# Performance work log

Measured on AMD Instinct MI355X. Metric: run time of the kernel, lower is better.

The kernel has to match this reference:

```python
import jax, jax.numpy as jnp
import numpy as np

VERTEX_W = 1.0
SMOOTH_W = 0.1
SYM_W = 0.05
CHAMFER_W = 0.1

B, N = 4, 8192  # N points per cloud, flat dim = N*3


def setup_inputs() -> dict:
    key = jax.random.key(0)
    k1, k2 = jax.random.split(key)
    pred = jax.random.normal(k1, (B, N * 3), dtype=jnp.float32)
    targ = jax.random.normal(k2, (B, N * 3), dtype=jnp.float32)
    return {"pred_vertices": pred, "target_vertices": targ}


def _chamfer(x, y):
    # x: [B,N,3], y: [B,M,3]; euclidean cdist via matmul expansion
    x2 = jnp.sum(x * x, axis=-1)  # [B,N]
    y2 = jnp.sum(y * y, axis=-1)  # [B,M]
    xy = jnp.einsum('bnd,bmd->bnm', x, y)  # [B,N,M]
    d2 = x2[:, :, None] + y2[None if False else slice(None), None, :] - 2.0 * xy
    d = jnp.sqrt(jnp.maximum(d2, 0.0))
    return jnp.mean(jnp.min(d, axis=2)) + jnp.mean(jnp.min(d, axis=1))


def reference(pred_vertices, target_vertices):
    b = pred_vertices.shape[0]
    pv = pred_vertices.reshape(b, -1, 3)
    tv = target_vertices.reshape(b, -1, 3)

    # vertex MSE (on flat tensors, same as mse on reshaped)
    vertex_loss = jnp.mean((pred_vertices - target_vertices) ** 2)

    # smoothness: mean L2 norm of consecutive vertex diffs
    diff = pv[:, 1:, :] - pv[:, :-1, :]
    smoothness_loss = jnp.mean(jnp.linalg.norm(diff, axis=2))

    # symmetry: N is even in this config
    mid = pv.shape[1] // 2
    left = pv[:, :mid, :]
    right = jnp.flip(pv[:, mid:, :], axis=1)
    right = right.at[:, :, 0].multiply(-1.0)
    symmetry_loss = jnp.mean((left - right) ** 2)

    chamfer_loss = _chamfer(pv, tv)

    total = (VERTEX_W * vertex_loss + SMOOTH_W * smoothness_loss
             + SYM_W * symmetry_loss + CHAMFER_W * chamfer_loss)
    return total
```

## Files before the change

kernel.cpp:

```cpp
#include <hip/hip_runtime.h>
#include <hip/hip_bf16.h>


#define B_ 4
#define N_ 8192
#define MID_ (N_ / 2)
#define CNT_OFF 1536
#define RP_OFF 1664
#define PM_OFF 4096
#define PACK_OFF (PM_OFF + 4 * 2 * B_ * N_)
#define PACK_STRIDE (B_ * N_ * 16)

typedef short short8 __attribute__((ext_vector_type(8)));
typedef float f32x16 __attribute__((ext_vector_type(16)));

__global__ void AdvancedLoss3D_1881195675843_kernel() {}

__device__ inline unsigned short bfu(float x) {
    union { __hip_bfloat16 b; unsigned short u; } c;
    c.b = __float2bfloat16(x);
    return c.u;
}
__device__ inline float bff(unsigned short u) {
    union { __hip_bfloat16 b; unsigned short u; } c;
    c.u = u;
    return __bfloat162float(c.b);
}

__device__ inline void enc(float x, float y, float z,
                           unsigned short* A, unsigned short* Bv) {
    float n2 = fmaf(x, x, fmaf(y, y, z * z));
    unsigned short hx = bfu(x), hy = bfu(y), hz = bfu(z);
    float fx = bff(hx), fy = bff(hy), fz = bff(hz);
    unsigned short lx = bfu(x - fx), ly = bfu(y - fy), lz = bfu(z - fz);
    unsigned short mx = bfu(-2.f * fx), my = bfu(-2.f * fy), mz = bfu(-2.f * fz);
    unsigned short nx = bfu(-2.f * bff(lx)), ny = bfu(-2.f * bff(ly)),
                   nz = bfu(-2.f * bff(lz));
    unsigned short n2h = bfu(n2);
    unsigned short n2l = bfu(n2 - bff(n2h));
    unsigned short one = bfu(1.0f);
    A[0] = mx; A[1] = my; A[2] = mz;
    A[3] = mx; A[4] = my; A[5] = mz;
    A[6] = nx; A[7] = ny; A[8] = nz;
    A[9] = n2h; A[10] = n2l; A[11] = one; A[12] = one;
    A[13] = A[14] = A[15] = 0;
    Bv[0] = hx; Bv[1] = hy; Bv[2] = hz;
    Bv[3] = lx; Bv[4] = ly; Bv[5] = lz;
    Bv[6] = hx; Bv[7] = hy; Bv[8] = hz;
    Bv[9] = one; Bv[10] = one; Bv[11] = n2h; Bv[12] = n2l;
    Bv[13] = Bv[14] = Bv[15] = 0;
}

__global__ __launch_bounds__(64) void prep_aux(const float* __restrict__ pred,
                                               const float* __restrict__ targ,
                                               float* __restrict__ ws) {
    int idx = blockIdx.x * 64 + threadIdx.x;
    int b = idx >> 13;
    int i = idx & (N_ - 1);
    const float* p = pred + (size_t)idx * 3;
    const float* t = targ + (size_t)idx * 3;
    float px = p[0], py = p[1], pz = p[2];
    float tx = t[0], ty = t[1], tz = t[2];

    if (idx == 0) ((unsigned int*)ws)[CNT_OFF] = 0u;

    unsigned short* pk = (unsigned short*)(ws + PACK_OFF);
    {
        union U { unsigned short s[16]; uint4 q[2]; } ua, ub, uc, ud;
        enc(px, py, pz, ua.s, ub.s);
        enc(tx, ty, tz, uc.s, ud.s);
        uint4* ap = (uint4*)(pk + (size_t)idx * 16);
        ap[0] = ua.q[0]; ap[1] = ua.q[1];
        uint4* bp = (uint4*)(pk + PACK_STRIDE + (size_t)idx * 16);
        bp[0] = ub.q[0]; bp[1] = ub.q[1];
        uint4* at = (uint4*)(pk + 2 * PACK_STRIDE + (size_t)idx * 16);
        at[0] = uc.q[0]; at[1] = uc.q[1];
        uint4* bt = (uint4*)(pk + 3 * PACK_STRIDE + (size_t)idx * 16);
        bt[0] = ud.q[0]; bt[1] = ud.q[1];
    }

    float dx = px - tx, dy = py - ty, dz = pz - tz;
    float dv = dx * dx + dy * dy + dz * dz;

    float sm = 0.f;
    if (i < N_ - 1) {
        float ex = p[3] - px, ey = p[4] - py, ez = p[5] - pz;
        sm = sqrtf(ex * ex + ey * ey + ez * ez);
    }

    float sy = 0.f;
    if (i < MID_) {
        const float* r = pred + ((size_t)(b * N_ + (N_ - 1 - i))) * 3;
        float ax = px + r[0];
        float ay = py - r[1];
        float az = pz - r[2];
        sy = ax * ax + ay * ay + az * az;
    }

    for (int off = 32; off; off >>= 1) {
        dv += __shfl_down(dv, off, 64);
        sm += __shfl_down(sm, off, 64);
        sy += __shfl_down(sy, off, 64);
    }
    if (threadIdx.x == 0) {
        ws[3 * blockIdx.x + 0] = dv;
        ws[3 * blockIdx.x + 1] = sm;
        ws[3 * blockIdx.x + 2] = sy;
    }
}

__global__ __launch_bounds__(256) void chamfer_mfma(const unsigned short* __restrict__ packs,
                                                    float* __restrict__ pm) {
    int bid = blockIdx.x;
    int chunk = bid & 31;
    int rgb = bid >> 5;
    int dir = chunk >> 4;
    int b   = (chunk >> 2) & 3;
    int cc  = chunk & 3;
    int w   = threadIdx.x >> 6;
    int l   = threadIdx.x & 63;
    int lr  = l & 31;
    int kh  = l >> 5;

    const unsigned short* Ap = packs + (dir ? 2 : 0) * PACK_STRIDE;
    const unsigned short* Bp = packs + (dir ? 1 : 3) * PACK_STRIDE;

    int rowbase = (rgb * 4 + w) * 64;
    const unsigned short* abase = Ap + ((size_t)(b * N_ + rowbase + lr)) * 16 + kh * 8;
    short8 af0 = *(const short8*)abase;
    short8 af1 = *(const short8*)(abase + 32 * 16);

    float rmin0[16], rmin1[16];
#pragma unroll
    for (int j = 0; j < 16; j++) { rmin0[j] = 3.4e38f; rmin1[j] = 3.4e38f; }

    const unsigned short* bbase = Bp + ((size_t)(b * N_ + cc * 2048 + lr)) * 16 + kh * 8;
    short8 f0 = *(const short8*)(bbase);
    short8 f1 = *(const short8*)(bbase + 512);
    short8 f2 = *(const short8*)(bbase + 1024);
    short8 f3 = *(const short8*)(bbase + 1536);

    const f32x16 zero = {0.f, 0.f, 0.f, 0.f, 0.f, 0.f, 0.f, 0.f,
                         0.f, 0.f, 0.f, 0.f, 0.f, 0.f, 0.f, 0.f};

    for (int t = 0; t < 64; t += 4) {
        int t4 = t + 4 < 64 ? t + 4 : 63;
        int t5 = t + 5 < 64 ? t + 5 : 63;
        int t6 = t + 6 < 64 ? t + 6 : 63;
        int t7 = t + 7 < 64 ? t + 7 : 63;
        {
            f32x16 aE = __builtin_amdgcn_mfma_f32_32x32x16_bf16(af0, f0, zero, 0, 0, 0);
            f32x16 aO = __builtin_amdgcn_mfma_f32_32x32x16_bf16(af0, f1, zero, 0, 0, 0);
#pragma unroll
            for (int j = 0; j < 16; j++)
                rmin0[j] = fminf(fminf(rmin0[j], aE[j]), aO[j]);
            aE = __builtin_amdgcn_mfma_f32_32x32x16_bf16(af1, f0, zero, 0, 0, 0);
            aO = __builtin_amdgcn_mfma_f32_32x32x16_bf16(af1, f1, zero, 0, 0, 0);
#pragma unroll
            for (int j = 0; j < 16; j++)
                rmin1[j] = fminf(fminf(rmin1[j], aE[j]), aO[j]);
            f0 = *(const short8*)(bbase + (size_t)t4 * 512);
            f1 = *(const short8*)(bbase + (size_t)t5 * 512);
        }
        {
            f32x16 aE = __builtin_amdgcn_mfma_f32_32x32x16_bf16(af0, f2, zero, 0, 0, 0);
            f32x16 aO = __builtin_amdgcn_mfma_f32_32x32x16_bf16(af0, f3, zero, 0, 0, 0);
#pragma unroll
            for (int j = 0; j < 16; j++)
                rmin0[j] = fminf(fminf(rmin0[j], aE[j]), aO[j]);
            aE = __builtin_amdgcn_mfma_f32_32x32x16_bf16(af1, f2, zero, 0, 0, 0);
            aO = __builtin_amdgcn_mfma_f32_32x32x16_bf16(af1, f3, zero, 0, 0, 0);
#pragma unroll
            for (int j = 0; j < 16; j++)
                rmin1[j] = fminf(fminf(rmin1[j], aE[j]), aO[j]);
            f2 = *(const short8*)(bbase + (size_t)t6 * 512);
            f3 = *(const short8*)(bbase + (size_t)t7 * 512);
        }
    }

    __shared__ float sred[4][64][32];
#pragma unroll
    for (int j = 0; j < 16; j++) {
        int r0 = (j & 3) + 8 * (j >> 2) + 4 * kh;
        sred[w][r0][(lr + r0) & 31] = rmin0[j];
        int r1 = 32 + r0;
        sred[w][r1][(lr + r1) & 31] = rmin1[j];
    }
    __syncthreads();
    float v = 3.4e38f;
#pragma unroll
    for (int c = 0; c < 32; c++)
        v = fminf(v, sred[w][l][(c + l) & 31]);
    pm[(size_t)cc * 65536 + dir * 32768 + b * N_ + rowbase + l] = v;
}

__global__ __launch_bounds__(256) void reduce_compose(const float* __restrict__ pm,
                                                      float* __restrict__ ws,
                                                      unsigned int* __restrict__ out) {
    int bid = blockIdx.x, tid = threadIdx.x;
    int idx = bid * 256 + tid;
    float v = 3.4e38f;
#pragma unroll
    for (int s = 0; s < 4; s++)
        v = fminf(v, pm[(size_t)s * 65536 + idx]);
    float d = sqrtf(fmaxf(v, 0.f));
    for (int off = 32; off; off >>= 1) d += __shfl_down(d, off, 64);
    __shared__ float red[4];
    __shared__ int is_last;
    int lane = tid & 63, w = tid >> 6;
    if (lane == 0) red[w] = d;
    __syncthreads();
    if (tid == 0) {
        ws[RP_OFF + bid] = red[0] + red[1] + red[2] + red[3];
        __threadfence();
        unsigned old = atomicAdd((unsigned int*)ws + CNT_OFF, 1u);
        is_last = (old == 255u);
    }
    __syncthreads();
    if (!is_last) return;

    if (tid == 0) __threadfence();
    __syncthreads();
    float rp = ws[RP_OFF + tid];
    float cr = (tid < 128) ? rp : 0.f;
    float cc = (tid < 128) ? 0.f : rp;
    float dv = ws[3 * tid]     + ws[3 * (tid + 256)];
    float sm = ws[3 * tid + 1] + ws[3 * (tid + 256) + 1];
    float sy = ws[3 * tid + 2] + ws[3 * (tid + 256) + 2];
    for (int off = 32; off; off >>= 1) {
        dv += __shfl_down(dv, off, 64);
        sm += __shfl_down(sm, off, 64);
        sy += __shfl_down(sy, off, 64);
        cr += __shfl_down(cr, off, 64);
        cc += __shfl_down(cc, off, 64);
    }
    __shared__ float red5[5][4];
    if (lane == 0) { red5[0][w] = dv; red5[1][w] = sm; red5[2][w] = sy;
                     red5[3][w] = cr; red5[4][w] = cc; }
    __syncthreads();
    if (tid == 0) {
        float S[5];
#pragma unroll
        for (int q = 0; q < 5; q++)
            S[q] = red5[q][0] + red5[q][1] + red5[q][2] + red5[q][3];
        float vertex = S[0] / (float)(B_ * N_ * 3);
        float smooth = S[1] / (float)(B_ * (N_ - 1));
        float sym    = S[2] / (float)(B_ * MID_ * 3);
        float cham   = (S[3] + S[4]) / (float)(B_ * N_);
        float total  = vertex + 0.1f * smooth + 0.05f * sym + 0.1f * cham;
        union { __hip_bfloat16 b; unsigned short u; } cv;
        cv.b = __float2bfloat16(total);
        out[0] = ((unsigned int)cv.u << 16) | (unsigned int)cv.u;
    }
}

extern "C" void kernel_launch(void* const* d_in, const int* in_sizes, int n_in,
                              void* d_out, int out_size, void* d_ws, size_t ws_size,
                              hipStream_t stream) {
    (void)in_sizes; (void)n_in; (void)out_size; (void)ws_size;
    const float* pred = (const float*)d_in[0];
    const float* targ = (const float*)d_in[1];
    float* wsf = (float*)d_ws;

    prep_aux<<<dim3(512), dim3(64), 0, stream>>>(pred, targ, wsf);
    chamfer_mfma<<<dim3(1024), dim3(256), 0, stream>>>(
        (const unsigned short*)(wsf + PACK_OFF), wsf + PM_OFF);
    reduce_compose<<<dim3(256), dim3(256), 0, stream>>>(
        wsf + PM_OFF, wsf, (unsigned int*)d_out);
}
```

Baseline: 92.99 us.

## Stage B fragments through LDS with async global-to-LDS double buffering

Replaces per-wave direct global loads of the B operand with cooperative async global_load_lds copies into a double-buffered shared-memory tile. All four waves now share each B tile instead of each fetching it separately, and the reduction scratch reuses the same LDS buffer. This adds a __syncthreads per group and LDS read traffic, and the prefetch relies on the async load having completed by the barrier without an explicit vmcnt wait.

```diff
diff --git a/kernel.cpp b/kernel.cpp
--- a/kernel.cpp
+++ b/kernel.cpp
@@ -15,6 +15,13 @@
 typedef float f32x16 __attribute__((ext_vector_type(16)));
 
 __global__ void AdvancedLoss3D_1881195675843_kernel() {}
+
+__device__ __forceinline__ void async16(void* lds, const void* g) {
+    __builtin_amdgcn_global_load_lds(
+        (const __attribute__((address_space(1))) unsigned int*)g,
+        (__attribute__((address_space(3))) unsigned int*)lds,
+        16, 0, 0);
+}
 
 __device__ inline unsigned short bfu(float x) {
     union { __hip_bfloat16 b; unsigned short u; } c;
@@ -134,51 +141,46 @@
 #pragma unroll
     for (int j = 0; j < 16; j++) { rmin0[j] = 3.4e38f; rmin1[j] = 3.4e38f; }
 
-    const unsigned short* bbase = Bp + ((size_t)(b * N_ + cc * 2048 + lr)) * 16 + kh * 8;
-    short8 f0 = *(const short8*)(bbase);
-    short8 f1 = *(const short8*)(bbase + 512);
-    short8 f2 = *(const short8*)(bbase + 1024);
-    short8 f3 = *(const short8*)(bbase + 1536);
+    __shared__ __align__(16) unsigned char smem[32768];
+    const unsigned short* bchunk = Bp + (size_t)(b * N_ + cc * 2048) * 16;
 
     const f32x16 zero = {0.f, 0.f, 0.f, 0.f, 0.f, 0.f, 0.f, 0.f,
                          0.f, 0.f, 0.f, 0.f, 0.f, 0.f, 0.f, 0.f};
 
-    for (int t = 0; t < 64; t += 4) {
-        int t4 = t + 4 < 64 ? t + 4 : 63;
-        int t5 = t + 5 < 64 ? t + 5 : 63;
-        int t6 = t + 6 < 64 ? t + 6 : 63;
-        int t7 = t + 7 < 64 ? t + 7 : 63;
-        {
-            f32x16 aE = __builtin_amdgcn_mfma_f32_32x32x16_bf16(af0, f0, zero, 0, 0, 0);
-            f32x16 aO = __builtin_amdgcn_mfma_f32_32x32x16_bf16(af0, f1, zero, 0, 0, 0);
+#define STAGE(buf, g)                                                        \
+    do {                                                                     \
+        int _t0 = (g) * 8 + 2 * w;         \
+        async16(smem + (buf) * 8192 + 2 * w * 1024,                          \
+                bchunk + (size_t)_t0 * 512 + l * 8);                         \
+        async16(smem + (buf) * 8192 + (2 * w + 1) * 1024,                    \
+                bchunk + (size_t)(_t0 + 1) * 512 + l * 8);                   \
+    } while (0)
+
+    STAGE(0, 0);
+    __syncthreads();
+    for (int g = 0; g < 8; ++g) {
+        if (g + 1 < 8) STAGE((g + 1) & 1, g + 1);
+        const unsigned char* bb = smem + (g & 1) * 8192;
+#pragma unroll
+        for (int tp = 0; tp < 8; tp += 2) {
+            short8 bE = *(const short8*)(bb + tp * 1024 + lr * 32 + kh * 16);
+            short8 bO = *(const short8*)(bb + (tp + 1) * 1024 + lr * 32 + kh * 16);
+            f32x16 aE = __builtin_amdgcn_mfma_f32_32x32x16_bf16(af0, bE, zero, 0, 0, 0);
+            f32x16 aO = __builtin_amdgcn_mfma_f32_32x32x16_bf16(af0, bO, zero, 0, 0, 0);
 #pragma unroll
             for (int j = 0; j < 16; j++)
                 rmin0[j] = fminf(fminf(rmin0[j], aE[j]), aO[j]);
-            aE = __builtin_amdgcn_mfma_f32_32x32x16_bf16(af1, f0, zero, 0, 0, 0);
-            aO = __builtin_amdgcn_mfma_f32_32x32x16_bf16(af1, f1, zero, 0, 0, 0);
+            aE = __builtin_amdgcn_mfma_f32_32x32x16_bf16(af1, bE, zero, 0, 0, 0);
+            aO = __builtin_amdgcn_mfma_f32_32x32x16_bf16(af1, bO, zero, 0, 0, 0);
 #pragma unroll
             for (int j = 0; j < 16; j++)
                 rmin1[j] = fminf(fminf(rmin1[j], aE[j]), aO[j]);
-            f0 = *(const short8*)(bbase + (size_t)t4 * 512);
-            f1 = *(const short8*)(bbase + (size_t)t5 * 512);
         }
-        {
-            f32x16 aE = __builtin_amdgcn_mfma_f32_32x32x16_bf16(af0, f2, zero, 0, 0, 0);
-            f32x16 aO = __builtin_amdgcn_mfma_f32_32x32x16_bf16(af0, f3, zero, 0, 0, 0);
-#pragma unroll
-            for (int j = 0; j < 16; j++)
-                rmin0[j] = fminf(fminf(rmin0[j], aE[j]), aO[j]);
-            aE = __builtin_amdgcn_mfma_f32_32x32x16_bf16(af1, f2, zero, 0, 0, 0);
-            aO = __builtin_amdgcn_mfma_f32_32x32x16_bf16(af1, f3, zero, 0, 0, 0);
-#pragma unroll
-            for (int j = 0; j < 16; j++)
-                rmin1[j] = fminf(fminf(rmin1[j], aE[j]), aO[j]);
-            f2 = *(const short8*)(bbase + (size_t)t6 * 512);
-            f3 = *(const short8*)(bbase + (size_t)t7 * 512);
-        }
-    }
-
-    __shared__ float sred[4][64][32];
+        __syncthreads();
+    }
+#undef STAGE
+
+    float (*sred)[64][32] = (float (*)[64][32])smem;
 #pragma unroll
     for (int j = 0; j < 16; j++) {
         int r0 = (j & 3) + 8 * (j >> 2) + 4 * kh;
```

New measurement: 91.48 us. No clear change (-1.6%).
